# Performance work log

Hardware: AMD Instinct MI355X
Metric: run time of the kernel (lower is better)

## Reference

```python
import jax, jax.numpy as jnp
import numpy as np
import math

B, L, D = 8, 2048, 1024   # batch, seq_len, d_in == d_hidden
A = 256                   # attn_dim = max(32, D // 4)


def setup_inputs() -> dict:
    key = jax.random.key(0)
    ks = jax.random.split(key, 6)
    s_in = 1.0 / math.sqrt(D)
    s_a = 1.0 / math.sqrt(A)
    return {
        "x": jax.random.normal(ks[0], (B, L, D), jnp.float32),
        "Wq": jax.random.normal(ks[1], (D, A), jnp.float32) * s_in,
        "Wk": jax.random.normal(ks[2], (D, A), jnp.float32) * s_in,
        "Wv": jax.random.normal(ks[3], (D, A), jnp.float32) * s_in,
        "Wu": jax.random.normal(ks[4], (A, 3 * D), jnp.float32) * s_a,
        "v_f": jax.random.normal(ks[5], (D,), jnp.float32) * 0.1,
        "v_r": jax.random.normal(jax.random.fold_in(key, 7), (D,), jnp.float32) * 0.1,
        "bias_f": jnp.zeros((D,), jnp.float32),
        "bias_r": jnp.zeros((D,), jnp.float32),
        "alpha": jnp.float32(0.5),
    }


def reference(x, Wq, Wk, Wv, Wu, v_f, v_r, bias_f, bias_r, alpha):
    # --- attention-augmented projection U (B, L, 3H) ---
    Q = jnp.einsum("bld,da->bla", x, Wq)
    K = jnp.einsum("bld,da->bla", x, Wk)
    V = jnp.einsum("bld,da->bla", x, Wv)
    logits = jnp.einsum("bqa,bka->bqk", Q, K) / jnp.sqrt(jnp.float32(Q.shape[-1]))
    attn = jax.nn.softmax(logits, axis=-1)
    F_attn = jnp.einsum("bqk,bka->bqa", attn, V)
    mixed = alpha * F_attn + Q
    U = jnp.einsum("bla,ah->blh", mixed, Wu)  # (B, L, 3H)
    u_f, u_r, u_h = jnp.split(U, 3, axis=-1)

    # --- SRU recurrence via scan over time ---
    c0 = jnp.zeros((x.shape[0], v_f.shape[0]), x.dtype)

    def step(c_prev, inp):
        uf_t, ur_t, uh_t, x_t = inp
        f_t = jax.nn.sigmoid(uf_t + v_f * c_prev + bias_f)
        c_t = f_t * c_prev + (1.0 - f_t) * uh_t
        r_t = jax.nn.sigmoid(ur_t + v_r * c_prev + bias_r)
        h_t = r_t * c_t + (1.0 - r_t) * x_t
        return c_t, h_t

    xs = (
        jnp.swapaxes(u_f, 0, 1),  # (L, B, H)
        jnp.swapaxes(u_r, 0, 1),
        jnp.swapaxes(u_h, 0, 1),
        jnp.swapaxes(x, 0, 1),
    )
    _, h_seq = jax.lax.scan(step, c0, xs)
    return jnp.swapaxes(h_seq, 0, 1)  # (B, L, H)
```

## Files before the change

kernel.cpp:

```cpp
#include <hip/hip_runtime.h>


typedef __attribute__((ext_vector_type(4))) float f32x4;
typedef __attribute__((ext_vector_type(8))) short bf16x8;
typedef __attribute__((ext_vector_type(8))) unsigned short u16x8;

__device__ __forceinline__ float b2f(unsigned short u) {
  union { unsigned int i; float f; } v; v.i = ((unsigned int)u) << 16; return v.f;
}
__device__ __forceinline__ unsigned short f2b(float f) {
  union { float f; unsigned int i; } v; v.f = f;
  unsigned int r = v.i + 0x7FFFu + ((v.i >> 16) & 1u);
  return (unsigned short)(r >> 16);
}

typedef __attribute__((address_space(3))) unsigned int lds_u32;
typedef __attribute__((address_space(1))) const unsigned int glb_u32;
__device__ __forceinline__ void gld_lds16(const void* g, void* l) {
  __builtin_amdgcn_global_load_lds((glb_u32*)g, (lds_u32*)l, 16, 0, 0);
}

__global__ __launch_bounds__(256) void k_conv_x(const float* __restrict__ x,
                                                unsigned short* __restrict__ xb) {
  size_t i = ((size_t)blockIdx.x * 256 + threadIdx.x) * 8;
  float4 a = *(const float4*)(x + i);
  float4 b = *(const float4*)(x + i + 4);
  u16x8 o;
  o[0] = f2b(a.x); o[1] = f2b(a.y); o[2] = f2b(a.z); o[3] = f2b(a.w);
  o[4] = f2b(b.x); o[5] = f2b(b.y); o[6] = f2b(b.z); o[7] = f2b(b.w);
  *(u16x8*)(xb + i) = o;
}

__global__ __launch_bounds__(256) void k_conv_w(const float* __restrict__ Wq,
                                                const float* __restrict__ Wk,
                                                const float* __restrict__ Wv,
                                                const float* __restrict__ Wu,
                                                unsigned short* __restrict__ wqkvT,
                                                unsigned short* __restrict__ wuT) {
  int id = blockIdx.x * 256 + threadIdx.x;
  if (id < 768 * 1024) {
    int n = id >> 10, k = id & 1023;
    float v;
    if (n < 256)      v = Wq[k * 256 + n];
    else if (n < 512) v = Wk[k * 256 + (n - 256)];
    else              v = Wv[k * 256 + (n - 512)];
    wqkvT[id] = f2b(v);
  } else {
    int id2 = id - 768 * 1024;
    int n = id2 >> 8, k = id2 & 255;
    wuT[id2] = f2b(Wu[k * 3072 + n]);
  }
}

__global__ __launch_bounds__(256) void k_gemm_bt(const unsigned short* __restrict__ A,
                                                 const unsigned short* __restrict__ B,
                                                 unsigned short* __restrict__ C,
                                                 int M, int N, int K) {
  __shared__ unsigned short As[128 * 32];
  __shared__ unsigned short Bs[128 * 32];
  const int tid = threadIdx.x;
  const int lane = tid & 63, wave = tid >> 6;
  const int m0 = blockIdx.y * 128, n0 = blockIdx.x * 128;
  const int wm = (wave >> 1) * 64, wn = (wave & 1) * 64;
  const int la = lane & 15, lg = lane >> 4;
  f32x4 acc[4][4] = {};
  const int r0 = tid >> 2;
  const int kk0 = (tid & 3) * 8;
  const unsigned short* Ag = A + (size_t)(m0 + r0) * K + kk0;
  const unsigned short* Bg = B + (size_t)(n0 + r0) * K + kk0;
  unsigned short* Al = As + tid * 8;
  unsigned short* Bl = Bs + tid * 8;

  for (int kt = 0; kt < K; kt += 32) {
    gld_lds16(Ag + kt, Al);
    gld_lds16(Ag + kt + (size_t)64 * K, Al + 2048);
    gld_lds16(Bg + kt, Bl);
    gld_lds16(Bg + kt + (size_t)64 * K, Bl + 2048);
    __syncthreads();
    bf16x8 af[4], bfr[4];
#pragma unroll
    for (int mt = 0; mt < 4; ++mt) af[mt]  = *(const bf16x8*)&As[(wm + mt * 16 + la) * 32 + lg * 8];
#pragma unroll
    for (int nt = 0; nt < 4; ++nt) bfr[nt] = *(const bf16x8*)&Bs[(wn + nt * 16 + la) * 32 + lg * 8];
#pragma unroll
    for (int mt = 0; mt < 4; ++mt)
#pragma unroll
      for (int nt = 0; nt < 4; ++nt)
        acc[mt][nt] = __builtin_amdgcn_mfma_f32_16x16x32_bf16(af[mt], bfr[nt], acc[mt][nt], 0, 0, 0);
    __syncthreads();
  }
#pragma unroll
  for (int mt = 0; mt < 4; ++mt)
#pragma unroll
    for (int nt = 0; nt < 4; ++nt)
#pragma unroll
      for (int i = 0; i < 4; ++i) {
        int row = m0 + wm + mt * 16 + lg * 4 + i;
        int col = n0 + wn + nt * 16 + la;
        C[(size_t)row * N + col] = f2b(acc[mt][nt][i]);
      }
}

__global__ __launch_bounds__(256) void k_transpose_v(const unsigned short* __restrict__ qkv,
                                                     unsigned short* __restrict__ vt) {
  __shared__ unsigned short tile[32][33];
  int b = blockIdx.z;
  int l0 = blockIdx.x * 32, n0 = blockIdx.y * 32;
  int tx = threadIdx.x, ty = threadIdx.y;
#pragma unroll
  for (int i = 0; i < 4; ++i) {
    int l = l0 + ty + i * 8;
    tile[ty + i * 8][tx] = qkv[(size_t)(b * 2048 + l) * 768 + 512 + n0 + tx];
  }
  __syncthreads();
#pragma unroll
  for (int i = 0; i < 4; ++i) {
    int n = n0 + ty + i * 8;
    vt[(size_t)(b * 256 + n) * 2048 + l0 + tx] = tile[tx][ty + i * 8];
  }
}

__global__ __launch_bounds__(256) void k_attn(const unsigned short* __restrict__ qkv,
                                              const unsigned short* __restrict__ vt,
                                              unsigned short* __restrict__ mixed,
                                              const float* __restrict__ alpha_p) {
  __shared__ unsigned short Ks[64][264];
  __shared__ unsigned short Vs[256][72];
  __shared__ unsigned short Ps[4][16][72];
  const int tid = threadIdx.x;
  const int lane = tid & 63, wave = tid >> 6;
  const int b = blockIdx.y;
  const int qw = blockIdx.x * 64 + wave * 16;
  const int la = lane & 15, lg = lane >> 4;
  const float alpha = *alpha_p;
  const float scale = 0.0625f;

  bf16x8 aq[8];
  {
    const unsigned short* qrow = qkv + (size_t)(b * 2048 + qw + la) * 768;
#pragma unroll
    for (int ks = 0; ks < 8; ++ks) aq[ks] = *(const bf16x8*)(qrow + ks * 32 + lg * 8);
  }
  f32x4 acc[16] = {};
  float mrun[4] = {-1e30f, -1e30f, -1e30f, -1e30f};
  float lrun[4] = {0.f, 0.f, 0.f, 0.f};

  for (int kc = 0; kc < 2048; kc += 64) {
    {
      const unsigned short* kg = qkv + (size_t)(b * 2048 + kc) * 768 + 256;
#pragma unroll
      for (int i = 0; i < 8; ++i) {
        int chunk = i * 256 + tid;
        int r = chunk >> 5, ci = chunk & 31;
        *(u16x8*)&Ks[r][ci * 8] = *(const u16x8*)(kg + (size_t)r * 768 + ci * 8);
      }
      const unsigned short* vg = vt + (size_t)(b * 256) * 2048 + kc;
#pragma unroll
      for (int i = 0; i < 8; ++i) {
        int chunk = i * 256 + tid;
        int n = chunk >> 3, ci = chunk & 7;
        *(u16x8*)&Vs[n][ci * 8] = *(const u16x8*)(vg + (size_t)n * 2048 + ci * 8);
      }
    }
    __syncthreads();
    f32x4 s[4] = {};
#pragma unroll
    for (int ks = 0; ks < 8; ++ks)
#pragma unroll
      for (int nt = 0; nt < 4; ++nt) {
        bf16x8 bk = *(const bf16x8*)&Ks[nt * 16 + la][ks * 32 + lg * 8];
        s[nt] = __builtin_amdgcn_mfma_f32_16x16x32_bf16(aq[ks], bk, s[nt], 0, 0, 0);
      }
    float sc_old[4], psum[4];
#pragma unroll
    for (int i = 0; i < 4; ++i) {
      float v = fmaxf(fmaxf(s[0][i], s[1][i]), fmaxf(s[2][i], s[3][i]));
#pragma unroll
      for (int off = 1; off < 16; off <<= 1) v = fmaxf(v, __shfl_xor(v, off, 64));
      v *= scale;
      float mn = fmaxf(mrun[i], v);
      sc_old[i] = __expf(mrun[i] - mn);
      mrun[i] = mn;
      psum[i] = 0.f;
    }
    float pv[4][4];
#pragma unroll
    for (int nt = 0; nt < 4; ++nt)
#pragma unroll
      for (int i = 0; i < 4; ++i) {
        float p = __expf(s[nt][i] * scale - mrun[i]);
        pv[nt][i] = p;
        psum[i] += p;
      }
#pragma unroll
    for (int i = 0; i < 4; ++i) {
      float v = psum[i];
#pragma unroll
      for (int off = 1; off < 16; off <<= 1) v += __shfl_xor(v, off, 64);
      lrun[i] = lrun[i] * sc_old[i] + v;
    }
#pragma unroll
    for (int on = 0; on < 16; ++on)
#pragma unroll
      for (int i = 0; i < 4; ++i) acc[on][i] *= sc_old[i];
#pragma unroll
    for (int nt = 0; nt < 4; ++nt)
#pragma unroll
      for (int i = 0; i < 4; ++i)
        Ps[wave][lg * 4 + i][nt * 16 + la] = f2b(pv[nt][i]);
    bf16x8 pa0 = *(const bf16x8*)&Ps[wave][la][lg * 8];
    bf16x8 pa1 = *(const bf16x8*)&Ps[wave][la][32 + lg * 8];
#pragma unroll
    for (int on = 0; on < 16; ++on) {
      bf16x8 bv0 = *(const bf16x8*)&Vs[on * 16 + la][lg * 8];
      bf16x8 bv1 = *(const bf16x8*)&Vs[on * 16 + la][32 + lg * 8];
      acc[on] = __builtin_amdgcn_mfma_f32_16x16x32_bf16(pa0, bv0, acc[on], 0, 0, 0);
      acc[on] = __builtin_amdgcn_mfma_f32_16x16x32_bf16(pa1, bv1, acc[on], 0, 0, 0);
    }
    __syncthreads();
  }
  float invl[4];
#pragma unroll
  for (int i = 0; i < 4; ++i) invl[i] = 1.f / lrun[i];
#pragma unroll
  for (int on = 0; on < 16; ++on)
#pragma unroll
    for (int i = 0; i < 4; ++i) {
      int row = b * 2048 + qw + lg * 4 + i;
      int col = on * 16 + la;
      float fa = acc[on][i] * invl[i];
      float qv = b2f(qkv[(size_t)row * 768 + col]);
      mixed[(size_t)row * 256 + col] = f2b(alpha * fa + qv);
    }
}

__global__ __launch_bounds__(64) void k_sru(const unsigned short* __restrict__ U,
                                            const float* __restrict__ x,
                                            const float* __restrict__ vf,
                                            const float* __restrict__ vr,
                                            const float* __restrict__ bfv,
                                            const float* __restrict__ brv,
                                            float* __restrict__ out) {
  constexpr int PF = 8;
  int idx = blockIdx.x * 64 + threadIdx.x;
  int b = idx >> 10, d = idx & 1023;
  const unsigned short* Ub = U + (size_t)b * 2048 * 3072 + d;
  const float* xb = x + (size_t)b * 2048 * 1024 + d;
  float* ob = out + (size_t)b * 2048 * 1024 + d;
  float c = 0.f;
  float vfd = vf[d], vrd = vr[d], bfd = bfv[d], brd = brv[d];

  float buf_uf[PF], buf_ur[PF], buf_uh[PF], buf_x[PF];
#pragma unroll
  for (int j = 0; j < PF; ++j) {
    buf_uf[j] = b2f(Ub[(size_t)j * 3072]);
    buf_ur[j] = b2f(Ub[(size_t)j * 3072 + 1024]);
    buf_uh[j] = b2f(Ub[(size_t)j * 3072 + 2048]);
    buf_x[j]  = xb[(size_t)j * 1024];
  }
  for (int tc = 0; tc < 2048; tc += PF) {
    float n_uf[PF], n_ur[PF], n_uh[PF], n_x[PF];
#pragma unroll
    for (int j = 0; j < PF; ++j) {
      int t = tc + PF + j; t = t < 2047 ? t : 2047;
      n_uf[j] = b2f(Ub[(size_t)t * 3072]);
      n_ur[j] = b2f(Ub[(size_t)t * 3072 + 1024]);
      n_uh[j] = b2f(Ub[(size_t)t * 3072 + 2048]);
      n_x[j]  = xb[(size_t)t * 1024];
    }
#pragma unroll
    for (int j = 0; j < PF; ++j) {
      float f = 1.f / (1.f + __expf(-(buf_uf[j] + vfd * c + bfd)));
      float cn = f * (c - buf_uh[j]) + buf_uh[j];
      float r = 1.f / (1.f + __expf(-(buf_ur[j] + vrd * c + brd)));
      ob[(size_t)(tc + j) * 1024] = r * (cn - buf_x[j]) + buf_x[j];
      c = cn;
    }
#pragma unroll
    for (int j = 0; j < PF; ++j) {
      buf_uf[j] = n_uf[j]; buf_ur[j] = n_ur[j];
      buf_uh[j] = n_uh[j]; buf_x[j]  = n_x[j];
    }
  }
}

extern "C" void kernel_launch(void* const* d_in, const int* in_sizes, int n_in,
                              void* d_out, int out_size, void* d_ws, size_t ws_size,
                              hipStream_t stream) {
  const float* x     = (const float*)d_in[0];
  const float* Wq    = (const float*)d_in[1];
  const float* Wk    = (const float*)d_in[2];
  const float* Wv    = (const float*)d_in[3];
  const float* Wu    = (const float*)d_in[4];
  const float* vf    = (const float*)d_in[5];
  const float* vr    = (const float*)d_in[6];
  const float* bf_   = (const float*)d_in[7];
  const float* br_   = (const float*)d_in[8];
  const float* alpha = (const float*)d_in[9];

  char* ws = (char*)d_ws;
  unsigned short* xb     = (unsigned short*)(ws);
  unsigned short* wqkvT  = (unsigned short*)(ws + 33554432);
  unsigned short* wuT    = (unsigned short*)(ws + 35127296);
  unsigned short* qkv    = (unsigned short*)(ws + 36700160);
  unsigned short* vt     = (unsigned short*)(ws + 61865984);
  unsigned short* mixedb = (unsigned short*)(ws + 70254592);
  unsigned short* Ub     = (unsigned short*)(ws + 78643200);
  float* out = (float*)d_out;

  k_conv_x<<<8192, 256, 0, stream>>>(x, xb);
  k_conv_w<<<6144, 256, 0, stream>>>(Wq, Wk, Wv, Wu, wqkvT, wuT);
  k_gemm_bt<<<dim3(6, 128), 256, 0, stream>>>(xb, wqkvT, qkv, 16384, 768, 1024);
  k_transpose_v<<<dim3(64, 8, 8), dim3(32, 8), 0, stream>>>(qkv, vt);
  k_attn<<<dim3(32, 8), 256, 0, stream>>>(qkv, vt, mixedb, alpha);
  k_gemm_bt<<<dim3(24, 128), 256, 0, stream>>>(mixedb, wuT, Ub, 16384, 3072, 256);
  k_sru<<<128, 64, 0, stream>>>(Ub, x, vf, vr, bf_, br_, out);
}
```

Before: 601.4 us.

## Store U in time-chunked layout and deepen SRU prefetch with vector loads

The U-projection GEMM now writes its output in a [b][gate][t/8][d][8] layout, so each SRU thread fetches 8 timesteps of each gate with one 16-byte load. The SRU kernel keeps a four-slot software pipeline of in-flight loads, issued with inline asm and gated by explicit vmcnt waits. It also switches to 32-thread blocks over 256 blocks to spread the serial scan across more CUs. The aim is to hide memory latency in the latency-bound recurrence. The cost is scattered 2-byte stores in the GEMM epilogue, and the hand-set waitcnt depends on the exact instruction count.

```diff
diff --git a/kernel.cpp b/kernel.cpp
--- a/kernel.cpp
+++ b/kernel.cpp
@@ -52,6 +52,7 @@
   }
 }
 
+template <int MODE>
 __global__ __launch_bounds__(256) void k_gemm_bt(const unsigned short* __restrict__ A,
                                                  const unsigned short* __restrict__ B,
                                                  unsigned short* __restrict__ C,
@@ -97,7 +98,14 @@
       for (int i = 0; i < 4; ++i) {
         int row = m0 + wm + mt * 16 + lg * 4 + i;
         int col = n0 + wn + nt * 16 + la;
-        C[(size_t)row * N + col] = f2b(acc[mt][nt][i]);
+        if constexpr (MODE == 0) {
+          C[(size_t)row * N + col] = f2b(acc[mt][nt][i]);
+        } else {
+          int bb = row >> 11, t = row & 2047;
+          int a = col >> 10, dd = col & 1023;
+          size_t off = (((size_t)(bb * 3 + a) * 256 + (t >> 3)) * 1024 + dd) * 8 + (t & 7);
+          C[off] = f2b(acc[mt][nt][i]);
+        }
       }
 }
 
@@ -234,6 +242,52 @@
     }
 }
 
+struct SruSlot {
+  u16x8 uf, ur, uh;
+  float xs[8];
+};
+
+__device__ __forceinline__ void sru_issue(SruSlot& s,
+                                          const unsigned short* Uf,
+                                          const unsigned short* Ur,
+                                          const unsigned short* Uh,
+                                          const float* xb, int cc) {
+  int tt = cc < 255 ? cc : 255;
+  const unsigned short* pf = Uf + (size_t)tt * 8192;
+  const unsigned short* pr = Ur + (size_t)tt * 8192;
+  const unsigned short* ph = Uh + (size_t)tt * 8192;
+  asm volatile("global_load_dwordx4 %0, %1, off" : "=v"(s.uf) : "v"(pf));
+  asm volatile("global_load_dwordx4 %0, %1, off" : "=v"(s.ur) : "v"(pr));
+  asm volatile("global_load_dwordx4 %0, %1, off" : "=v"(s.uh) : "v"(ph));
+  const float* px = xb + (size_t)tt * 8192;
+#pragma unroll
+  for (int j = 0; j < 8; ++j)
+    asm volatile("global_load_dword %0, %1, off" : "=v"(s.xs[j]) : "v"(px + j * 1024));
+}
+
+__device__ __forceinline__ void sru_compute(const SruSlot& s, float& c,
+                                            float vfd, float vrd, float bfd, float brd,
+                                            float* ob, int cc) {
+#pragma unroll
+  for (int j = 0; j < 8; ++j) {
+    float uf = b2f((unsigned short)s.uf[j]);
+    float ur = b2f((unsigned short)s.ur[j]);
+    float uh = b2f((unsigned short)s.uh[j]);
+    float xt = s.xs[j];
+    float f = 1.f / (1.f + __expf(-(uf + vfd * c + bfd)));
+    float cn = f * (c - uh) + uh;
+    float r = 1.f / (1.f + __expf(-(ur + vrd * c + brd)));
+    ob[(size_t)(cc * 8 + j) * 1024] = r * (cn - xt) + xt;
+    c = cn;
+  }
+}
+
+#define SRU_WAIT()                                      \
+  do {                                                  \
+    asm volatile("s_waitcnt vmcnt(33)" ::: "memory");   \
+    __builtin_amdgcn_sched_barrier(0);                  \
+  } while (0)
+
 __global__ __launch_bounds__(64) void k_sru(const unsigned short* __restrict__ U,
                                             const float* __restrict__ x,
                                             const float* __restrict__ vf,
@@ -241,46 +295,26 @@
                                             const float* __restrict__ bfv,
                                             const float* __restrict__ brv,
                                             float* __restrict__ out) {
-  constexpr int PF = 8;
-  int idx = blockIdx.x * 64 + threadIdx.x;
+  int idx = blockIdx.x * 32 + threadIdx.x;
   int b = idx >> 10, d = idx & 1023;
-  const unsigned short* Ub = U + (size_t)b * 2048 * 3072 + d;
+  const unsigned short* Uf = U + ((size_t)(b * 3 + 0) << 21) + d * 8;
+  const unsigned short* Ur = U + ((size_t)(b * 3 + 1) << 21) + d * 8;
+  const unsigned short* Uh = U + ((size_t)(b * 3 + 2) << 21) + d * 8;
   const float* xb = x + (size_t)b * 2048 * 1024 + d;
   float* ob = out + (size_t)b * 2048 * 1024 + d;
   float c = 0.f;
   float vfd = vf[d], vrd = vr[d], bfd = bfv[d], brd = brv[d];
 
-  float buf_uf[PF], buf_ur[PF], buf_uh[PF], buf_x[PF];
-#pragma unroll
-  for (int j = 0; j < PF; ++j) {
-    buf_uf[j] = b2f(Ub[(size_t)j * 3072]);
-    buf_ur[j] = b2f(Ub[(size_t)j * 3072 + 1024]);
-    buf_uh[j] = b2f(Ub[(size_t)j * 3072 + 2048]);
-    buf_x[j]  = xb[(size_t)j * 1024];
-  }
-  for (int tc = 0; tc < 2048; tc += PF) {
-    float n_uf[PF], n_ur[PF], n_uh[PF], n_x[PF];
-#pragma unroll
-    for (int j = 0; j < PF; ++j) {
-      int t = tc + PF + j; t = t < 2047 ? t : 2047;
-      n_uf[j] = b2f(Ub[(size_t)t * 3072]);
-      n_ur[j] = b2f(Ub[(size_t)t * 3072 + 1024]);
-      n_uh[j] = b2f(Ub[(size_t)t * 3072 + 2048]);
-      n_x[j]  = xb[(size_t)t * 1024];
-    }
-#pragma unroll
-    for (int j = 0; j < PF; ++j) {
-      float f = 1.f / (1.f + __expf(-(buf_uf[j] + vfd * c + bfd)));
-      float cn = f * (c - buf_uh[j]) + buf_uh[j];
-      float r = 1.f / (1.f + __expf(-(buf_ur[j] + vrd * c + brd)));
-      ob[(size_t)(tc + j) * 1024] = r * (cn - buf_x[j]) + buf_x[j];
-      c = cn;
-    }
-#pragma unroll
-    for (int j = 0; j < PF; ++j) {
-      buf_uf[j] = n_uf[j]; buf_ur[j] = n_ur[j];
-      buf_uh[j] = n_uh[j]; buf_x[j]  = n_x[j];
-    }
+  SruSlot s0, s1, s2, s3;
+  sru_issue(s0, Uf, Ur, Uh, xb, 0);
+  sru_issue(s1, Uf, Ur, Uh, xb, 1);
+  sru_issue(s2, Uf, Ur, Uh, xb, 2);
+  sru_issue(s3, Uf, Ur, Uh, xb, 3);
+  for (int base = 0; base < 256; base += 4) {
+    SRU_WAIT(); sru_compute(s0, c, vfd, vrd, bfd, brd, ob, base + 0); sru_issue(s0, Uf, Ur, Uh, xb, base + 4);
+    SRU_WAIT(); sru_compute(s1, c, vfd, vrd, bfd, brd, ob, base + 1); sru_issue(s1, Uf, Ur, Uh, xb, base + 5);
+    SRU_WAIT(); sru_compute(s2, c, vfd, vrd, bfd, brd, ob, base + 2); sru_issue(s2, Uf, Ur, Uh, xb, base + 6);
+    SRU_WAIT(); sru_compute(s3, c, vfd, vrd, bfd, brd, ob, base + 3); sru_issue(s3, Uf, Ur, Uh, xb, base + 7);
   }
 }
 
@@ -310,9 +344,9 @@
 
   k_conv_x<<<8192, 256, 0, stream>>>(x, xb);
   k_conv_w<<<6144, 256, 0, stream>>>(Wq, Wk, Wv, Wu, wqkvT, wuT);
-  k_gemm_bt<<<dim3(6, 128), 256, 0, stream>>>(xb, wqkvT, qkv, 16384, 768, 1024);
+  k_gemm_bt<0><<<dim3(6, 128), 256, 0, stream>>>(xb, wqkvT, qkv, 16384, 768, 1024);
   k_transpose_v<<<dim3(64, 8, 8), dim3(32, 8), 0, stream>>>(qkv, vt);
   k_attn<<<dim3(32, 8), 256, 0, stream>>>(qkv, vt, mixedb, alpha);
-  k_gemm_bt<<<dim3(24, 128), 256, 0, stream>>>(mixedb, wuT, Ub, 16384, 3072, 256);
-  k_sru<<<128, 64, 0, stream>>>(Ub, x, vf, vr, bf_, br_, out);
-}
+  k_gemm_bt<1><<<dim3(24, 128), 256, 0, stream>>>(mixedb, wuT, Ub, 16384, 3072, 256);
+  k_sru<<<256, 32, 0, stream>>>(Ub, x, vf, vr, bf_, br_, out);
+}
```

After: 571.8 us. -4.9%, faster.
